# Kernel tuning notes

Hardware: AMD Instinct MI355X
Metric: run time of the kernel (lower is better)

The kernel has to match this reference:

```python
import jax, jax.numpy as jnp
import numpy as np

EPS = 1e-12  # F.normalize default eps


def setup_inputs() -> dict:
    key = jax.random.key(0)
    ks = jax.random.split(key, 6)
    B, C, D, H, W = 8, 192, 24, 24, 24
    heads = 6
    x = jax.random.normal(ks[0], (B, C, D, H, W), dtype=jnp.float32)
    qkv_w = jax.random.normal(ks[1], (3 * C, C), dtype=jnp.float32) * (1.0 / np.sqrt(C))
    qkv_b = jax.random.normal(ks[2], (3 * C,), dtype=jnp.float32) * 0.02
    temperature = jnp.ones((heads, 1, 1), dtype=jnp.float32)
    proj_w = jax.random.normal(ks[3], (C, C), dtype=jnp.float32) * (1.0 / np.sqrt(C))
    proj_b = jax.random.normal(ks[4], (C,), dtype=jnp.float32) * 0.02
    return {"x": x, "qkv_w": qkv_w, "qkv_b": qkv_b, "temperature": temperature,
            "proj_w": proj_w, "proj_b": proj_b}


def _l2norm_lastdim(t):
    n = jnp.sqrt(jnp.sum(t * t, axis=-1, keepdims=True))
    return t / jnp.maximum(n, EPS)


def reference(x, qkv_w, qkv_b, temperature, proj_w, proj_b):
    B, C, D, H, W = x.shape
    N = D * H * W
    heads = temperature.shape[0]
    hd = C // heads
    xf = x.reshape(B, C, N)
    # 1x1x1 Conv3d == per-voxel linear over channels: (B, 3C, N)
    qkv = jnp.einsum('bcn,oc->bon', xf, qkv_w) + qkv_b[None, :, None]
    # Faithful torch reshape of contiguous (B, 3C, N) buffer -> (B, N, 3, heads, hd),
    # then permute(2,0,3,4,1) -> (3, B, heads, hd, N)
    qkv = qkv.reshape(B, N, 3, heads, hd).transpose(2, 0, 3, 4, 1)
    q, k, v = qkv[0], qkv[1], qkv[2]
    q = _l2norm_lastdim(q)
    k = _l2norm_lastdim(k)
    # channel cross-covariance attention: (B, heads, hd, hd)
    attn = jnp.einsum('bhcn,bhdn->bhcd', q, k) * temperature[None]
    attn = jax.nn.softmax(attn, axis=-1)
    out = jnp.einsum('bhcd,bhdn->bhcn', attn, v)          # (B, heads, hd, N)
    out = out.transpose(0, 2, 1, 3).reshape(B, C, D, H, W)  # transpose(1,2) + reshape
    outf = out.reshape(B, C, N)
    y = jnp.einsum('bcn,oc->bon', outf, proj_w) + proj_b[None, :, None]
    return y.reshape(B, C, D, H, W)
```

## Files before the change

kernel.cpp:

```cpp
#include <hip/hip_runtime.h>

#define B_ 8
#define C_ 192
#define N_ 13824
#define HEADS 6
#define HD 32
#define THREEC 576

typedef unsigned short ushort_t;
typedef unsigned int uint_t;
typedef __attribute__((ext_vector_type(8))) short short8;
typedef __attribute__((ext_vector_type(4))) float f32x4;

__device__ __forceinline__ float bf2f(ushort_t u) {
  union { uint_t u; float f; } c; c.u = ((uint_t)u) << 16; return c.f;
}
__device__ __forceinline__ ushort_t f2bf(float f) {
  union { float f; uint_t u; } c; c.f = f;
  uint_t u = c.u;
  uint_t r = (u + 0x7fffu + ((u >> 16) & 1u)) >> 16;
  return (ushort_t)r;
}

#define LROW 200

__device__ __forceinline__ void rowperm(int f, int& row, int& u) {
  row = f / 24;
  int ul = f - row * 24;
  int uu = ul - (row & 7);
  u = uu + ((uu < 0) ? 24 : 0);
}

__global__ __launch_bounds__(256) void wconv(const float* __restrict__ w,
                                             ushort_t* __restrict__ wbf) {
  int idx = (blockIdx.x * 256 + threadIdx.x) * 8;
  float4 v0 = *(const float4*)&w[idx];
  float4 v1 = *(const float4*)&w[idx + 4];
  union { ushort_t us[8]; uint4 v; } pk;
  pk.us[0] = f2bf(v0.x); pk.us[1] = f2bf(v0.y); pk.us[2] = f2bf(v0.z); pk.us[3] = f2bf(v0.w);
  pk.us[4] = f2bf(v1.x); pk.us[5] = f2bf(v1.y); pk.us[6] = f2bf(v1.z); pk.us[7] = f2bf(v1.w);
  *(uint4*)&wbf[idx] = pk.v;
}

__global__ __launch_bounds__(256) void xt_conv(const float* __restrict__ x,
                                               ushort_t* __restrict__ xT) {
  __shared__ ushort_t tile[64 * 200];
  int t = threadIdx.x;
  int n0 = blockIdx.x * 64, b = blockIdx.y;
  const float* xb = x + (size_t)b * C_ * N_;
  int n4 = t & 15, cp = t >> 4;
#pragma unroll
  for (int it = 0; it < 6; ++it) {
    int c = (cp + it * 16) * 2;
    float4 v0 = *(const float4*)&xb[(size_t)c * N_ + n0 + n4 * 4];
    float4 v1 = *(const float4*)&xb[(size_t)(c + 1) * N_ + n0 + n4 * 4];
    float a0[4] = {v0.x, v0.y, v0.z, v0.w};
    float a1[4] = {v1.x, v1.y, v1.z, v1.w};
#pragma unroll
    for (int i = 0; i < 4; ++i) {
      uint_t wd = (uint_t)f2bf(a0[i]) | ((uint_t)f2bf(a1[i]) << 16);
      *(uint_t*)&tile[(n4 * 4 + i) * 200 + c] = wd;
    }
  }
  __syncthreads();
  ushort_t* xTb = xT + ((size_t)b * N_ + n0) * C_;
  int r = t >> 2, q = t & 3;
#pragma unroll
  for (int j = 0; j < 6; ++j) {
    int chunk = q * 6 + j;
    uint4 v = *(const uint4*)&tile[r * 200 + chunk * 8];
    *(uint4*)&xTb[r * 192 + chunk * 8] = v;
  }
}

__global__ __launch_bounds__(256) void qkv_gemm_mfma(
    const ushort_t* __restrict__ wbf, const ushort_t* __restrict__ xT,
    const float* __restrict__ bias, ushort_t* __restrict__ qkv) {
  __shared__ ushort_t As[64 * LROW];
  __shared__ ushort_t Bs[128 * LROW];
  int t = threadIdx.x;
  int o0 = blockIdx.x * 64, n0 = blockIdx.y * 128, b = blockIdx.z;
  int w = t >> 6, lane = t & 63;
  int ln16 = lane & 15, q4 = lane >> 4;

  const ushort_t* Asrc = wbf + (size_t)o0 * C_;
  const ushort_t* Bsrc = xT + ((size_t)b * N_ + n0) * C_;

  uint4 breg2[12]; int brow[12], bu[12];
#pragma unroll
  for (int j = 0; j < 12; ++j) {
    int f = (w * 12 + j) * 64 + lane;
    rowperm(f, brow[j], bu[j]);
    breg2[j] = *(const uint4*)(Bsrc + brow[j] * C_ + bu[j] * 8);
  }
  uint4 areg[6]; int arow[6], au[6];
#pragma unroll
  for (int j = 0; j < 6; ++j) {
    int f = (w * 6 + j) * 64 + lane;
    rowperm(f, arow[j], au[j]);
    areg[j] = *(const uint4*)(Asrc + arow[j] * C_ + au[j] * 8);
  }
#pragma unroll
  for (int j = 0; j < 12; ++j)
    *(uint4*)&Bs[brow[j] * LROW + bu[j] * 8] = breg2[j];
#pragma unroll
  for (int j = 0; j < 6; ++j)
    *(uint4*)&As[arow[j] * LROW + au[j] * 8] = areg[j];

  float breg[2][4];
#pragma unroll
  for (int mi = 0; mi < 2; ++mi)
#pragma unroll
    for (int r = 0; r < 4; ++r)
      breg[mi][r] = bias[o0 + (w >> 1) * 32 + mi * 16 + q4 * 4 + r];

  f32x4 acc[2][4];
#pragma unroll
  for (int mi = 0; mi < 2; ++mi)
#pragma unroll
    for (int ni = 0; ni < 4; ++ni) acc[mi][ni] = (f32x4){0.f, 0.f, 0.f, 0.f};

  __syncthreads();

  int mrow = (w >> 1) * 32, ncol = (w & 1) * 64;
#pragma unroll
  for (int kk = 0; kk < 6; ++kk) {
    int k0 = kk * 32 + q4 * 8;
    short8 a[2], bb[4];
#pragma unroll
    for (int mi = 0; mi < 2; ++mi)
      a[mi] = *(const short8*)&As[(mrow + mi * 16 + ln16) * LROW + k0];
#pragma unroll
    for (int ni = 0; ni < 4; ++ni)
      bb[ni] = *(const short8*)&Bs[(ncol + ni * 16 + ln16) * LROW + k0];
#pragma unroll
    for (int mi = 0; mi < 2; ++mi)
#pragma unroll
      for (int ni = 0; ni < 4; ++ni)
        acc[mi][ni] = __builtin_amdgcn_mfma_f32_16x16x32_bf16(
            a[mi], bb[ni], acc[mi][ni], 0, 0, 0);
  }

#pragma unroll
  for (int mi = 0; mi < 2; ++mi)
#pragma unroll
    for (int ni = 0; ni < 4; ++ni)
#pragma unroll
      for (int r = 0; r < 4; ++r) {
        float v = acc[mi][ni][r] + breg[mi][r];
        uint_t bf = f2bf(v);
        uint_t pv = (uint_t)__shfl_xor((int)bf, 1);
        if (!(lane & 1)) {
          int o_l = mrow + mi * 16 + q4 * 4 + r;
          int n_l = ncol + ni * 16 + ln16;
          *(uint_t*)&qkv[(size_t)(b * THREEC + o0 + o_l) * N_ + n0 + n_l] =
              bf | (pv << 16);
        }
      }
}

__global__ __launch_bounds__(256) void attn_partial(
    const ushort_t* __restrict__ qkv, float* __restrict__ Spart) {
  __shared__ float sh[4608];
  int t = threadIdx.x;
  int chunk = blockIdx.x, h = blockIdx.y, b = blockIdx.z;
  int j = t & 31, g8 = t >> 5;
  int tg = t >> 6, tl = t & 63;
  int c0 = (tl & 7) * 4, d0 = (tl >> 3) * 4;
  float acc[4][4];
#pragma unroll
  for (int i = 0; i < 4; ++i)
#pragma unroll
    for (int m = 0; m < 4; ++m) acc[i][m] = 0.f;
  float sqq = 0.f, sqk = 0.f;
  const ushort_t* basep = qkv + (size_t)b * THREEC * N_;
  int n2base = chunk * 1728;

  for (int p = 0; p < 27; ++p) {
    __syncthreads();
#pragma unroll
    for (int i = 0; i < 8; ++i) {
      int n2l = g8 * 8 + i;
      int n2 = n2base + p * 64 + n2l;
      int o = n2 / 24, r = n2 - o * 24;
      const ushort_t* rp = basep + (size_t)o * N_ + r * THREEC + h * HD + j;
      float qv = bf2f(rp[0]);
      float kv = bf2f(rp[C_]);
      sh[n2l * 32 + j] = qv;
      sh[2048 + n2l * 32 + j] = kv;
      sqq = fmaf(qv, qv, sqq);
      sqk = fmaf(kv, kv, sqk);
    }
    __syncthreads();
#pragma unroll
    for (int i = 0; i < 16; ++i) {
      int n2l = tg * 16 + i;
      float4 q4 = *(const float4*)&sh[n2l * 32 + c0];
      float4 k4 = *(const float4*)&sh[2048 + n2l * 32 + d0];
      float q[4] = {q4.x, q4.y, q4.z, q4.w};
      float kk[4] = {k4.x, k4.y, k4.z, k4.w};
#pragma unroll
      for (int ii = 0; ii < 4; ++ii)
#pragma unroll
        for (int mm = 0; mm < 4; ++mm)
          acc[ii][mm] = fmaf(q[ii], kk[mm], acc[ii][mm]);
    }
  }
  __syncthreads();
#pragma unroll
  for (int ii = 0; ii < 4; ++ii)
#pragma unroll
    for (int mm = 0; mm < 4; ++mm)
      sh[tg * 1024 + (c0 + ii) * 32 + (d0 + mm)] = acc[ii][mm];
  sh[4096 + g8 * 32 + j] = sqq;
  sh[4352 + g8 * 32 + j] = sqk;
  __syncthreads();

  float* outp = Spart + (size_t)((b * HEADS + h) * 8 + chunk) * 1088;
  for (int e = t; e < 1024; e += 256)
    outp[e] = sh[e] + sh[1024 + e] + sh[2048 + e] + sh[3072 + e];
  if (t < 32) {
    float s = 0.f;
#pragma unroll
    for (int g = 0; g < 8; ++g) s += sh[4096 + g * 32 + t];
    outp[1024 + t] = s;
  } else if (t < 64) {
    int jj = t - 32;
    float s = 0.f;
#pragma unroll
    for (int g = 0; g < 8; ++g) s += sh[4352 + g * 32 + jj];
    outp[1056 + jj] = s;
  }
}

__global__ __launch_bounds__(256) void attn_final(
    const float* __restrict__ Spart, const float* __restrict__ temp,
    const float* __restrict__ proj_w, ushort_t* __restrict__ W2bf) {
  __shared__ float Sl[1024];
  __shared__ float invq[32], invk[32];
  __shared__ float Pl[192 * 33];
  int t = threadIdx.x;
  int h = blockIdx.x, b = blockIdx.y;
  const float* base = Spart + (size_t)((b * HEADS + h) * 8) * 1088;

  for (int e = t; e < 1024; e += 256) {
    float s = 0.f;
#pragma unroll
    for (int ch = 0; ch < 8; ++ch) s += base[ch * 1088 + e];
    Sl[e] = s;
  }
  if (t < 64) {
    int jj = t & 31;
    int off = 1024 + (t >> 5) * 32 + jj;
    float s = 0.f;
#pragma unroll
    for (int ch = 0; ch < 8; ++ch) s += base[ch * 1088 + off];
    float inv = 1.f / fmaxf(sqrtf(s), 1e-12f);
    if (t < 32) invq[jj] = inv; else invk[jj] = inv;
  }
  for (int e = t; e < 6144; e += 256) {
    int co = e >> 5, c = e & 31;
    Pl[co * 33 + c] = proj_w[(size_t)co * C_ + c * HEADS + h];
  }
  __syncthreads();

  {
    int c = t >> 3, l8 = t & 7;
    float tmpv = temp[h];
    float iq = invq[c];
    float lg[4];
#pragma unroll
    for (int m = 0; m < 4; ++m) {
      int d = l8 * 4 + m;
      lg[m] = Sl[c * 32 + d] * iq * invk[d] * tmpv;
    }
    float mx = fmaxf(fmaxf(lg[0], lg[1]), fmaxf(lg[2], lg[3]));
    for (int off = 1; off < 8; off <<= 1) mx = fmaxf(mx, __shfl_xor(mx, off, 8));
    float ex[4]; float ssum = 0.f;
#pragma unroll
    for (int m = 0; m < 4; ++m) { ex[m] = __expf(lg[m] - mx); ssum += ex[m]; }
    for (int off = 1; off < 8; off <<= 1) ssum += __shfl_xor(ssum, off, 8);
    float inv = 1.f / ssum;
#pragma unroll
    for (int m = 0; m < 4; ++m) Sl[c * 32 + l8 * 4 + m] = ex[m] * inv;
  }
  __syncthreads();

  for (int e2 = t; e2 < 6144; e2 += 256) {
    int co = e2 >> 5, d = e2 & 31;
    float s = 0.f;
#pragma unroll
    for (int c = 0; c < 32; ++c)
      s = fmaf(Pl[co * 33 + c], Sl[c * 32 + d], s);
    W2bf[((size_t)b * C_ + co) * C_ + h * HD + d] = f2bf(s);
  }
}

__global__ __launch_bounds__(256) void proj_mfma(
    const ushort_t* __restrict__ qkv, const ushort_t* __restrict__ W2bf,
    const float* __restrict__ pb, float* __restrict__ y) {
  __shared__ ushort_t As[64 * LROW];
  __shared__ ushort_t Bs[128 * LROW];
  int t = threadIdx.x;
  int o0 = blockIdx.x * 64, n2_0 = blockIdx.y * 128, b = blockIdx.z;
  int w = t >> 6, lane = t & 63;
  int ln16 = lane & 15, q4 = lane >> 4;

  const ushort_t* Asrc = W2bf + ((size_t)b * C_ + o0) * C_;
  const ushort_t* basep = qkv + (size_t)b * THREEC * N_;

  uint4 breg2[12]; int brow[12], bu[12];
#pragma unroll
  for (int j = 0; j < 12; ++j) {
    int f = (w * 12 + j) * 64 + lane;
    rowperm(f, brow[j], bu[j]);
    int n2 = n2_0 + brow[j];
    int o = n2 / 24, r2 = n2 - o * 24;
    breg2[j] = *(const uint4*)(basep + (size_t)o * N_ + r2 * THREEC + 384 + bu[j] * 8);
  }
  uint4 areg[6]; int arow[6], au[6];
#pragma unroll
  for (int j = 0; j < 6; ++j) {
    int f = (w * 6 + j) * 64 + lane;
    rowperm(f, arow[j], au[j]);
    areg[j] = *(const uint4*)(Asrc + arow[j] * C_ + au[j] * 8);
  }
#pragma unroll
  for (int j = 0; j < 12; ++j)
    *(uint4*)&Bs[brow[j] * LROW + bu[j] * 8] = breg2[j];
#pragma unroll
  for (int j = 0; j < 6; ++j)
    *(uint4*)&As[arow[j] * LROW + au[j] * 8] = areg[j];

  float breg[2][4];
#pragma unroll
  for (int mi = 0; mi < 2; ++mi)
#pragma unroll
    for (int r = 0; r < 4; ++r)
      breg[mi][r] = pb[o0 + (w >> 1) * 32 + mi * 16 + q4 * 4 + r];

  f32x4 acc[2][4];
#pragma unroll
  for (int mi = 0; mi < 2; ++mi)
#pragma unroll
    for (int ni = 0; ni < 4; ++ni) acc[mi][ni] = (f32x4){0.f, 0.f, 0.f, 0.f};

  __syncthreads();

  int mrow = (w >> 1) * 32, ncol = (w & 1) * 64;
#pragma unroll
  for (int kk = 0; kk < 6; ++kk) {
    int k0 = kk * 32 + q4 * 8;
    short8 a[2], bb[4];
#pragma unroll
    for (int mi = 0; mi < 2; ++mi)
      a[mi] = *(const short8*)&As[(mrow + mi * 16 + ln16) * LROW + k0];
#pragma unroll
    for (int ni = 0; ni < 4; ++ni)
      bb[ni] = *(const short8*)&Bs[(ncol + ni * 16 + ln16) * LROW + k0];
#pragma unroll
    for (int mi = 0; mi < 2; ++mi)
#pragma unroll
      for (int ni = 0; ni < 4; ++ni)
        acc[mi][ni] = __builtin_amdgcn_mfma_f32_16x16x32_bf16(
            a[mi], bb[ni], acc[mi][ni], 0, 0, 0);
  }

#pragma unroll
  for (int mi = 0; mi < 2; ++mi)
#pragma unroll
    for (int ni = 0; ni < 4; ++ni)
#pragma unroll
      for (int r = 0; r < 4; ++r) {
        int co_l = mrow + mi * 16 + q4 * 4 + r;
        int n_l = ncol + ni * 16 + ln16;
        y[((size_t)b * C_ + o0 + co_l) * N_ + n2_0 + n_l] =
            acc[mi][ni][r] + breg[mi][r];
      }
}

extern "C" void kernel_launch(void* const* d_in, const int* in_sizes, int n_in,
                              void* d_out, int out_size, void* d_ws, size_t ws_size,
                              hipStream_t stream) {
  const float* x      = (const float*)d_in[0];
  const float* qkv_w  = (const float*)d_in[1];
  const float* qkv_b  = (const float*)d_in[2];
  const float* temp   = (const float*)d_in[3];
  const float* proj_w = (const float*)d_in[4];
  const float* proj_b = (const float*)d_in[5];
  float* y = (float*)d_out;

  char* wp = (char*)d_ws;
  ushort_t* qkv  = (ushort_t*)wp;  wp += (size_t)B_ * THREEC * N_ * 2;
  ushort_t* xT   = (ushort_t*)wp;  wp += (size_t)B_ * N_ * C_ * 2;
  float* Spart   = (float*)wp;     wp += (size_t)B_ * HEADS * 8 * 1088 * 4;
  ushort_t* W2bf = (ushort_t*)wp;  wp += (size_t)B_ * C_ * C_ * 2;
  ushort_t* wbf  = (ushort_t*)wp;

  wconv<<<54, 256, 0, stream>>>(qkv_w, wbf);
  xt_conv<<<dim3(216, B_), 256, 0, stream>>>(x, xT);
  qkv_gemm_mfma<<<dim3(9, 108, B_), 256, 0, stream>>>(wbf, xT, qkv_b, qkv);
  attn_partial<<<dim3(8, HEADS, B_), 256, 0, stream>>>(qkv, Spart);
  attn_final<<<dim3(HEADS, B_), 256, 0, stream>>>(Spart, temp, proj_w, W2bf);
  proj_mfma<<<dim3(3, 108, B_), 256, 0, stream>>>(qkv, W2bf, proj_b, y);
}
```

Before: 339.7 us.

## Fuse bf16 conversion into QKV GEMM, loop output tiles, and rework attention partials

The separate weight and input bf16 conversion kernels are removed. The QKV GEMM now reads fp32 x directly, converts it into LDS, and keeps the B fragments in registers while looping over all nine output-channel tiles, prefetching the next weight tile. Attention partial sums are restructured to handle all heads per block with 54 chunks, coalesced uint4 loads and double-buffered bf16 LDS. The projection GEMM likewise loops over output tiles and reuses the B fragments. This drops the xT round trip and several launches, at the cost of higher register pressure and fewer, longer blocks.

```diff
diff --git a/kernel.cpp b/kernel.cpp
--- a/kernel.cpp
+++ b/kernel.cpp
@@ -6,6 +6,7 @@
 #define HEADS 6
 #define HD 32
 #define THREEC 576
+#define CH 54
 
 typedef unsigned short ushort_t;
 typedef unsigned int uint_t;
@@ -14,6 +15,12 @@
 
 __device__ __forceinline__ float bf2f(ushort_t u) {
   union { uint_t u; float f; } c; c.u = ((uint_t)u) << 16; return c.f;
+}
+__device__ __forceinline__ float lo_f(uint_t u) {
+  union { uint_t u; float f; } c; c.u = u << 16; return c.f;
+}
+__device__ __forceinline__ float hi_f(uint_t u) {
+  union { uint_t u; float f; } c; c.u = u & 0xffff0000u; return c.f;
 }
 __device__ __forceinline__ ushort_t f2bf(float f) {
   union { float f; uint_t u; } c; c.f = f;
@@ -24,212 +31,215 @@
 
 #define LROW 200
 
-__device__ __forceinline__ void rowperm(int f, int& row, int& u) {
-  row = f / 24;
-  int ul = f - row * 24;
-  int uu = ul - (row & 7);
-  u = uu + ((uu < 0) ? 24 : 0);
-}
-
-__global__ __launch_bounds__(256) void wconv(const float* __restrict__ w,
-                                             ushort_t* __restrict__ wbf) {
-  int idx = (blockIdx.x * 256 + threadIdx.x) * 8;
-  float4 v0 = *(const float4*)&w[idx];
-  float4 v1 = *(const float4*)&w[idx + 4];
-  union { ushort_t us[8]; uint4 v; } pk;
-  pk.us[0] = f2bf(v0.x); pk.us[1] = f2bf(v0.y); pk.us[2] = f2bf(v0.z); pk.us[3] = f2bf(v0.w);
-  pk.us[4] = f2bf(v1.x); pk.us[5] = f2bf(v1.y); pk.us[6] = f2bf(v1.z); pk.us[7] = f2bf(v1.w);
-  *(uint4*)&wbf[idx] = pk.v;
-}
-
-__global__ __launch_bounds__(256) void xt_conv(const float* __restrict__ x,
-                                               ushort_t* __restrict__ xT) {
-  __shared__ ushort_t tile[64 * 200];
+__global__ __launch_bounds__(256, 2) void qkv_fused(
+    const float* __restrict__ x, const float* __restrict__ w,
+    const float* __restrict__ bias, ushort_t* __restrict__ qkv) {
+  __shared__ ushort_t Bs[128 * LROW];
+  __shared__ ushort_t As[64 * LROW];
   int t = threadIdx.x;
-  int n0 = blockIdx.x * 64, b = blockIdx.y;
+  int n0 = blockIdx.x * 128, b = blockIdx.y;
+  int wid = t >> 6, lane = t & 63;
+  int ln16 = lane & 15, q4 = lane >> 4;
   const float* xb = x + (size_t)b * C_ * N_;
-  int n4 = t & 15, cp = t >> 4;
-#pragma unroll
-  for (int it = 0; it < 6; ++it) {
-    int c = (cp + it * 16) * 2;
-    float4 v0 = *(const float4*)&xb[(size_t)c * N_ + n0 + n4 * 4];
-    float4 v1 = *(const float4*)&xb[(size_t)(c + 1) * N_ + n0 + n4 * 4];
-    float a0[4] = {v0.x, v0.y, v0.z, v0.w};
-    float a1[4] = {v1.x, v1.y, v1.z, v1.w};
-#pragma unroll
-    for (int i = 0; i < 4; ++i) {
-      uint_t wd = (uint_t)f2bf(a0[i]) | ((uint_t)f2bf(a1[i]) << 16);
-      *(uint_t*)&tile[(n4 * 4 + i) * 200 + c] = wd;
-    }
-  }
-  __syncthreads();
-  ushort_t* xTb = xT + ((size_t)b * N_ + n0) * C_;
-  int r = t >> 2, q = t & 3;
+
+  {
+    int nl = t & 127;
+    int cb0 = (t >> 7) * 8;
+#pragma unroll
+    for (int it = 0; it < 12; ++it) {
+      int cb = cb0 + it * 16;
+      float v[8];
+#pragma unroll
+      for (int j = 0; j < 8; ++j)
+        v[j] = xb[(size_t)(cb + j) * N_ + n0 + nl];
+      union { ushort_t us[8]; uint4 u4; } pk;
+#pragma unroll
+      for (int j = 0; j < 8; ++j) pk.us[j] = f2bf(v[j]);
+      *(uint4*)&Bs[nl * LROW + cb] = pk.u4;
+    }
+  }
+
+  int ar = t >> 2, au0 = t & 3;
+  uint4 apre[6];
 #pragma unroll
   for (int j = 0; j < 6; ++j) {
-    int chunk = q * 6 + j;
-    uint4 v = *(const uint4*)&tile[r * 200 + chunk * 8];
-    *(uint4*)&xTb[r * 192 + chunk * 8] = v;
-  }
-}
-
-__global__ __launch_bounds__(256) void qkv_gemm_mfma(
-    const ushort_t* __restrict__ wbf, const ushort_t* __restrict__ xT,
-    const float* __restrict__ bias, ushort_t* __restrict__ qkv) {
-  __shared__ ushort_t As[64 * LROW];
-  __shared__ ushort_t Bs[128 * LROW];
+    int u = au0 + 4 * j;
+    const float* src = w + (size_t)ar * C_ + u * 8;
+    float4 v0 = *(const float4*)src;
+    float4 v1 = *(const float4*)(src + 4);
+    union { ushort_t us[8]; uint4 u4; } pk;
+    pk.us[0] = f2bf(v0.x); pk.us[1] = f2bf(v0.y); pk.us[2] = f2bf(v0.z); pk.us[3] = f2bf(v0.w);
+    pk.us[4] = f2bf(v1.x); pk.us[5] = f2bf(v1.y); pk.us[6] = f2bf(v1.z); pk.us[7] = f2bf(v1.w);
+    apre[j] = pk.u4;
+  }
+
+  __syncthreads();
+
+#pragma unroll
+  for (int j = 0; j < 6; ++j)
+    *(uint4*)&As[ar * LROW + (au0 + 4 * j) * 8] = apre[j];
+
+  int ncol = (wid & 1) * 64, mrow = (wid >> 1) * 32;
+  short8 bb[6][4];
+#pragma unroll
+  for (int kk = 0; kk < 6; ++kk)
+#pragma unroll
+    for (int ni = 0; ni < 4; ++ni)
+      bb[kk][ni] = *(const short8*)&Bs[(ncol + ni * 16 + ln16) * LROW + kk * 32 + q4 * 8];
+
+  __syncthreads();
+
+  for (int p = 0; p < 9; ++p) {
+    if (p < 8) {
+      int o0n = (p + 1) * 64;
+#pragma unroll
+      for (int j = 0; j < 6; ++j) {
+        int u = au0 + 4 * j;
+        const float* src = w + (size_t)(o0n + ar) * C_ + u * 8;
+        float4 v0 = *(const float4*)src;
+        float4 v1 = *(const float4*)(src + 4);
+        union { ushort_t us[8]; uint4 u4; } pk;
+        pk.us[0] = f2bf(v0.x); pk.us[1] = f2bf(v0.y); pk.us[2] = f2bf(v0.z); pk.us[3] = f2bf(v0.w);
+        pk.us[4] = f2bf(v1.x); pk.us[5] = f2bf(v1.y); pk.us[6] = f2bf(v1.z); pk.us[7] = f2bf(v1.w);
+        apre[j] = pk.u4;
+      }
+    }
+
+    float brg[2][4];
+#pragma unroll
+    for (int mi = 0; mi < 2; ++mi)
+#pragma unroll
+      for (int r = 0; r < 4; ++r)
+        brg[mi][r] = bias[p * 64 + mrow + mi * 16 + q4 * 4 + r];
+
+    f32x4 acc[2][4];
+#pragma unroll
+    for (int mi = 0; mi < 2; ++mi)
+#pragma unroll
+      for (int ni = 0; ni < 4; ++ni) acc[mi][ni] = (f32x4){0.f, 0.f, 0.f, 0.f};
+
+#pragma unroll
+    for (int kk = 0; kk < 6; ++kk) {
+      short8 a[2];
+#pragma unroll
+      for (int mi = 0; mi < 2; ++mi)
+        a[mi] = *(const short8*)&As[(mrow + mi * 16 + ln16) * LROW + kk * 32 + q4 * 8];
+#pragma unroll
+      for (int mi = 0; mi < 2; ++mi)
+#pragma unroll
+        for (int ni = 0; ni < 4; ++ni)
+          acc[mi][ni] = __builtin_amdgcn_mfma_f32_16x16x32_bf16(
+              a[mi], bb[kk][ni], acc[mi][ni], 0, 0, 0);
+    }
+
+#pragma unroll
+    for (int mi = 0; mi < 2; ++mi)
+#pragma unroll
+      for (int ni = 0; ni < 4; ++ni)
+#pragma unroll
+        for (int r = 0; r < 4; ++r) {
+          float v = acc[mi][ni][r] + brg[mi][r];
+          uint_t bf = f2bf(v);
+          uint_t pv = (uint_t)__shfl_xor((int)bf, 1);
+          if (!(lane & 1)) {
+            int o_l = p * 64 + mrow + mi * 16 + q4 * 4 + r;
+            int n_l = ncol + ni * 16 + ln16;
+            *(uint_t*)&qkv[(size_t)(b * THREEC + o_l) * N_ + n0 + n_l] =
+                bf | (pv << 16);
+          }
+        }
+
+    __syncthreads();
+    if (p < 8) {
+#pragma unroll
+      for (int j = 0; j < 6; ++j)
+        *(uint4*)&As[ar * LROW + (au0 + 4 * j) * 8] = apre[j];
+      __syncthreads();
+    }
+  }
+}
+
+#define K2RS 392
+__global__ __launch_bounds__(384) void attn_partial(
+    const ushort_t* __restrict__ qkv, float* __restrict__ Spart) {
+  __shared__ ushort_t sh[2][32 * K2RS];
   int t = threadIdx.x;
-  int o0 = blockIdx.x * 64, n0 = blockIdx.y * 128, b = blockIdx.z;
-  int w = t >> 6, lane = t & 63;
-  int ln16 = lane & 15, q4 = lane >> 4;
-
-  const ushort_t* Asrc = wbf + (size_t)o0 * C_;
-  const ushort_t* Bsrc = xT + ((size_t)b * N_ + n0) * C_;
-
-  uint4 breg2[12]; int brow[12], bu[12];
-#pragma unroll
-  for (int j = 0; j < 12; ++j) {
-    int f = (w * 12 + j) * 64 + lane;
-    rowperm(f, brow[j], bu[j]);
-    breg2[j] = *(const uint4*)(Bsrc + brow[j] * C_ + bu[j] * 8);
-  }
-  uint4 areg[6]; int arow[6], au[6];
-#pragma unroll
-  for (int j = 0; j < 6; ++j) {
-    int f = (w * 6 + j) * 64 + lane;
-    rowperm(f, arow[j], au[j]);
-    areg[j] = *(const uint4*)(Asrc + arow[j] * C_ + au[j] * 8);
-  }
-#pragma unroll
-  for (int j = 0; j < 12; ++j)
-    *(uint4*)&Bs[brow[j] * LROW + bu[j] * 8] = breg2[j];
-#pragma unroll
-  for (int j = 0; j < 6; ++j)
-    *(uint4*)&As[arow[j] * LROW + au[j] * 8] = areg[j];
-
-  float breg[2][4];
-#pragma unroll
-  for (int mi = 0; mi < 2; ++mi)
-#pragma unroll
-    for (int r = 0; r < 4; ++r)
-      breg[mi][r] = bias[o0 + (w >> 1) * 32 + mi * 16 + q4 * 4 + r];
-
-  f32x4 acc[2][4];
-#pragma unroll
-  for (int mi = 0; mi < 2; ++mi)
-#pragma unroll
-    for (int ni = 0; ni < 4; ++ni) acc[mi][ni] = (f32x4){0.f, 0.f, 0.f, 0.f};
-
-  __syncthreads();
-
-  int mrow = (w >> 1) * 32, ncol = (w & 1) * 64;
-#pragma unroll
-  for (int kk = 0; kk < 6; ++kk) {
-    int k0 = kk * 32 + q4 * 8;
-    short8 a[2], bb[4];
-#pragma unroll
-    for (int mi = 0; mi < 2; ++mi)
-      a[mi] = *(const short8*)&As[(mrow + mi * 16 + ln16) * LROW + k0];
-#pragma unroll
-    for (int ni = 0; ni < 4; ++ni)
-      bb[ni] = *(const short8*)&Bs[(ncol + ni * 16 + ln16) * LROW + k0];
-#pragma unroll
-    for (int mi = 0; mi < 2; ++mi)
-#pragma unroll
-      for (int ni = 0; ni < 4; ++ni)
-        acc[mi][ni] = __builtin_amdgcn_mfma_f32_16x16x32_bf16(
-            a[mi], bb[ni], acc[mi][ni], 0, 0, 0);
-  }
-
-#pragma unroll
-  for (int mi = 0; mi < 2; ++mi)
-#pragma unroll
-    for (int ni = 0; ni < 4; ++ni)
-#pragma unroll
-      for (int r = 0; r < 4; ++r) {
-        float v = acc[mi][ni][r] + breg[mi][r];
-        uint_t bf = f2bf(v);
-        uint_t pv = (uint_t)__shfl_xor((int)bf, 1);
-        if (!(lane & 1)) {
-          int o_l = mrow + mi * 16 + q4 * 4 + r;
-          int n_l = ncol + ni * 16 + ln16;
-          *(uint_t*)&qkv[(size_t)(b * THREEC + o0 + o_l) * N_ + n0 + n_l] =
-              bf | (pv << 16);
-        }
+  int chunk = blockIdx.x, b = blockIdx.y;
+  const ushort_t* basep = qkv + (size_t)b * THREEC * N_;
+  int n2base = chunk * 256;
+  int h = t / 64, tl = t & 63;
+  int c0 = (tl & 7) * 4, d0 = (tl >> 3) * 4;
+
+  float acc[4][4];
+#pragma unroll
+  for (int i = 0; i < 4; ++i)
+#pragma unroll
+    for (int m = 0; m < 4; ++m) acc[i][m] = 0.f;
+  float sqq[4] = {0.f, 0.f, 0.f, 0.f}, sqk[4] = {0.f, 0.f, 0.f, 0.f};
+
+  uint4 pre[4];
+  int srr[4], sru[4];
+#pragma unroll
+  for (int i = 0; i < 4; ++i) {
+    int idx = t + i * 384;
+    srr[i] = idx / 48; sru[i] = idx - srr[i] * 48;
+  }
+#pragma unroll
+  for (int i = 0; i < 4; ++i) {
+    int n2 = n2base + srr[i];
+    int o = n2 / 24, rr = n2 - o * 24;
+    pre[i] = *(const uint4*)(basep + (size_t)o * N_ + rr * THREEC + sru[i] * 8);
+  }
+#pragma unroll
+  for (int i = 0; i < 4; ++i)
+    *(uint4*)&sh[0][srr[i] * K2RS + sru[i] * 8] = pre[i];
+
+  for (int it = 0; it < 8; ++it) {
+    if (it < 7) {
+#pragma unroll
+      for (int i = 0; i < 4; ++i) {
+        int n2 = n2base + (it + 1) * 32 + srr[i];
+        int o = n2 / 24, rr = n2 - o * 24;
+        pre[i] = *(const uint4*)(basep + (size_t)o * N_ + rr * THREEC + sru[i] * 8);
       }
-}
-
-__global__ __launch_bounds__(256) void attn_partial(
-    const ushort_t* __restrict__ qkv, float* __restrict__ Spart) {
-  __shared__ float sh[4608];
-  int t = threadIdx.x;
-  int chunk = blockIdx.x, h = blockIdx.y, b = blockIdx.z;
-  int j = t & 31, g8 = t >> 5;
-  int tg = t >> 6, tl = t & 63;
-  int c0 = (tl & 7) * 4, d0 = (tl >> 3) * 4;
-  float acc[4][4];
-#pragma unroll
-  for (int i = 0; i < 4; ++i)
-#pragma unroll
-    for (int m = 0; m < 4; ++m) acc[i][m] = 0.f;
-  float sqq = 0.f, sqk = 0.f;
-  const ushort_t* basep = qkv + (size_t)b * THREEC * N_;
-  int n2base = chunk * 1728;
-
-  for (int p = 0; p < 27; ++p) {
+    }
     __syncthreads();
-#pragma unroll
-    for (int i = 0; i < 8; ++i) {
-      int n2l = g8 * 8 + i;
-      int n2 = n2base + p * 64 + n2l;
-      int o = n2 / 24, r = n2 - o * 24;
-      const ushort_t* rp = basep + (size_t)o * N_ + r * THREEC + h * HD + j;
-      float qv = bf2f(rp[0]);
-      float kv = bf2f(rp[C_]);
-      sh[n2l * 32 + j] = qv;
-      sh[2048 + n2l * 32 + j] = kv;
-      sqq = fmaf(qv, qv, sqq);
-      sqk = fmaf(kv, kv, sqk);
-    }
-    __syncthreads();
-#pragma unroll
-    for (int i = 0; i < 16; ++i) {
-      int n2l = tg * 16 + i;
-      float4 q4 = *(const float4*)&sh[n2l * 32 + c0];
-      float4 k4 = *(const float4*)&sh[2048 + n2l * 32 + d0];
-      float q[4] = {q4.x, q4.y, q4.z, q4.w};
-      float kk[4] = {k4.x, k4.y, k4.z, k4.w};
-#pragma unroll
-      for (int ii = 0; ii < 4; ++ii)
-#pragma unroll
-        for (int mm = 0; mm < 4; ++mm)
-          acc[ii][mm] = fmaf(q[ii], kk[mm], acc[ii][mm]);
-    }
-  }
-  __syncthreads();
-#pragma unroll
-  for (int ii = 0; ii < 4; ++ii)
-#pragma unroll
-    for (int mm = 0; mm < 4; ++mm)
-      sh[tg * 1024 + (c0 + ii) * 32 + (d0 + mm)] = acc[ii][mm];
-  sh[4096 + g8 * 32 + j] = sqq;
-  sh[4352 + g8 * 32 + j] = sqk;
-  __syncthreads();
-
-  float* outp = Spart + (size_t)((b * HEADS + h) * 8 + chunk) * 1088;
-  for (int e = t; e < 1024; e += 256)
-    outp[e] = sh[e] + sh[1024 + e] + sh[2048 + e] + sh[3072 + e];
-  if (t < 32) {
-    float s = 0.f;
-#pragma unroll
-    for (int g = 0; g < 8; ++g) s += sh[4096 + g * 32 + t];
-    outp[1024 + t] = s;
-  } else if (t < 64) {
-    int jj = t - 32;
-    float s = 0.f;
-#pragma unroll
-    for (int g = 0; g < 8; ++g) s += sh[4352 + g * 32 + jj];
-    outp[1056 + jj] = s;
+    if (it < 7) {
+#pragma unroll
+      for (int i = 0; i < 4; ++i)
+        *(uint4*)&sh[(it + 1) & 1][srr[i] * K2RS + sru[i] * 8] = pre[i];
+    }
+    const ushort_t* buf = sh[it & 1];
+#pragma unroll 4
+    for (int row = 0; row < 32; ++row) {
+      uint2 qv = *(const uint2*)&buf[row * K2RS + h * HD + c0];
+      uint2 kv = *(const uint2*)&buf[row * K2RS + C_ + h * HD + d0];
+      float q[4] = {lo_f(qv.x), hi_f(qv.x), lo_f(qv.y), hi_f(qv.y)};
+      float k[4] = {lo_f(kv.x), hi_f(kv.x), lo_f(kv.y), hi_f(kv.y)};
+#pragma unroll
+      for (int i = 0; i < 4; ++i) {
+        sqq[i] = fmaf(q[i], q[i], sqq[i]);
+        sqk[i] = fmaf(k[i], k[i], sqk[i]);
+#pragma unroll
+        for (int m = 0; m < 4; ++m)
+          acc[i][m] = fmaf(q[i], k[m], acc[i][m]);
+      }
+    }
+  }
+
+  float* outp = Spart + ((size_t)(b * HEADS + h) * CH + chunk) * 1088;
+#pragma unroll
+  for (int i = 0; i < 4; ++i) {
+    float4 v = {acc[i][0], acc[i][1], acc[i][2], acc[i][3]};
+    *(float4*)&outp[(c0 + i) * 32 + d0] = v;
+  }
+  if (tl < 8) {
+#pragma unroll
+    for (int i = 0; i < 4; ++i) outp[1024 + c0 + i] = sqq[i];
+  }
+  if ((tl & 7) == 0) {
+#pragma unroll
+    for (int i = 0; i < 4; ++i) outp[1056 + d0 + i] = sqk[i];
   }
 }
 
@@ -241,20 +251,18 @@
   __shared__ float Pl[192 * 33];
   int t = threadIdx.x;
   int h = blockIdx.x, b = blockIdx.y;
-  const float* base = Spart + (size_t)((b * HEADS + h) * 8) * 1088;
+  const float* base = Spart + (size_t)(b * HEADS + h) * CH * 1088;
 
   for (int e = t; e < 1024; e += 256) {
     float s = 0.f;
-#pragma unroll
-    for (int ch = 0; ch < 8; ++ch) s += base[ch * 1088 + e];
+    for (int ch = 0; ch < CH; ++ch) s += base[ch * 1088 + e];
     Sl[e] = s;
   }
   if (t < 64) {
     int jj = t & 31;
     int off = 1024 + (t >> 5) * 32 + jj;
     float s = 0.f;
-#pragma unroll
-    for (int ch = 0; ch < 8; ++ch) s += base[ch * 1088 + off];
+    for (int ch = 0; ch < CH; ++ch) s += base[ch * 1088 + off];
     float inv = 1.f / fmaxf(sqrtf(s), 1e-12f);
     if (t < 32) invq[jj] = inv; else invk[jj] = inv;
   }
@@ -296,87 +304,109 @@
   }
 }
 
-__global__ __launch_bounds__(256) void proj_mfma(
+__global__ __launch_bounds__(256, 2) void proj_fused(
     const ushort_t* __restrict__ qkv, const ushort_t* __restrict__ W2bf,
     const float* __restrict__ pb, float* __restrict__ y) {
+  __shared__ ushort_t Bs[128 * LROW];
   __shared__ ushort_t As[64 * LROW];
-  __shared__ ushort_t Bs[128 * LROW];
   int t = threadIdx.x;
-  int o0 = blockIdx.x * 64, n2_0 = blockIdx.y * 128, b = blockIdx.z;
-  int w = t >> 6, lane = t & 63;
+  int n2_0 = blockIdx.x * 128, b = blockIdx.y;
+  int wid = t >> 6, lane = t & 63;
   int ln16 = lane & 15, q4 = lane >> 4;
-
-  const ushort_t* Asrc = W2bf + ((size_t)b * C_ + o0) * C_;
   const ushort_t* basep = qkv + (size_t)b * THREEC * N_;
 
-  uint4 breg2[12]; int brow[12], bu[12];
-#pragma unroll
-  for (int j = 0; j < 12; ++j) {
-    int f = (w * 12 + j) * 64 + lane;
-    rowperm(f, brow[j], bu[j]);
-    int n2 = n2_0 + brow[j];
-    int o = n2 / 24, r2 = n2 - o * 24;
-    breg2[j] = *(const uint4*)(basep + (size_t)o * N_ + r2 * THREEC + 384 + bu[j] * 8);
-  }
-  uint4 areg[6]; int arow[6], au[6];
+  {
+    int nl = t >> 1, u0 = t & 1;
+#pragma unroll
+    for (int j = 0; j < 12; ++j) {
+      int u = u0 + 2 * j;
+      int n2 = n2_0 + nl;
+      int o = n2 / 24, r2 = n2 - o * 24;
+      uint4 v = *(const uint4*)(basep + (size_t)o * N_ + r2 * THREEC + 384 + u * 8);
+      *(uint4*)&Bs[nl * LROW + u * 8] = v;
+    }
+  }
+
+  int ar = t >> 2, au0 = t & 3;
+  uint4 apre[6];
 #pragma unroll
   for (int j = 0; j < 6; ++j) {
-    int f = (w * 6 + j) * 64 + lane;
-    rowperm(f, arow[j], au[j]);
-    areg[j] = *(const uint4*)(Asrc + arow[j] * C_ + au[j] * 8);
-  }
-#pragma unroll
-  for (int j = 0; j < 12; ++j)
-    *(uint4*)&Bs[brow[j] * LROW + bu[j] * 8] = breg2[j];
+    int u = au0 + 4 * j;
+    apre[j] = *(const uint4*)(W2bf + ((size_t)b * C_ + ar) * C_ + u * 8);
+  }
+
+  __syncthreads();
+
 #pragma unroll
   for (int j = 0; j < 6; ++j)
-    *(uint4*)&As[arow[j] * LROW + au[j] * 8] = areg[j];
-
-  float breg[2][4];
-#pragma unroll
-  for (int mi = 0; mi < 2; ++mi)
-#pragma unroll
-    for (int r = 0; r < 4; ++r)
-      breg[mi][r] = pb[o0 + (w >> 1) * 32 + mi * 16 + q4 * 4 + r];
-
-  f32x4 acc[2][4];
-#pragma unroll
-  for (int mi = 0; mi < 2; ++mi)
-#pragma unroll
-    for (int ni = 0; ni < 4; ++ni) acc[mi][ni] = (f32x4){0.f, 0.f, 0.f, 0.f};
-
-  __syncthreads();
-
-  int mrow = (w >> 1) * 32, ncol = (w & 1) * 64;
-#pragma unroll
-  for (int kk = 0; kk < 6; ++kk) {
-    int k0 = kk * 32 + q4 * 8;
-    short8 a[2], bb[4];
-#pragma unroll
-    for (int mi = 0; mi < 2; ++mi)
-      a[mi] = *(const short8*)&As[(mrow + mi * 16 + ln16) * LROW + k0];
+    *(uint4*)&As[ar * LROW + (au0 + 4 * j) * 8] = apre[j];
+
+  int ncol = (wid & 1) * 64, mrow = (wid >> 1) * 32;
+  short8 bb[6][4];
+#pragma unroll
+  for (int kk = 0; kk < 6; ++kk)
 #pragma unroll
     for (int ni = 0; ni < 4; ++ni)
-      bb[ni] = *(const short8*)&Bs[(ncol + ni * 16 + ln16) * LROW + k0];
+      bb[kk][ni] = *(const short8*)&Bs[(ncol + ni * 16 + ln16) * LROW + kk * 32 + q4 * 8];
+
+  __syncthreads();
+
+  for (int p = 0; p < 3; ++p) {
+    if (p < 2) {
+      int o0n = (p + 1) * 64;
+#pragma unroll
+      for (int j = 0; j < 6; ++j) {
+        int u = au0 + 4 * j;
+        apre[j] = *(const uint4*)(W2bf + ((size_t)b * C_ + o0n + ar) * C_ + u * 8);
+      }
+    }
+
+    float brg[2][4];
+#pragma unroll
+    for (int mi = 0; mi < 2; ++mi)
+#pragma unroll
+      for (int r = 0; r < 4; ++r)
+        brg[mi][r] = pb[p * 64 + mrow + mi * 16 + q4 * 4 + r];
+
+    f32x4 acc[2][4];
+#pragma unroll
+    for (int mi = 0; mi < 2; ++mi)
+#pragma unroll
+      for (int ni = 0; ni < 4; ++ni) acc[mi][ni] = (f32x4){0.f, 0.f, 0.f, 0.f};
+
+#pragma unroll
+    for (int kk = 0; kk < 6; ++kk) {
+      short8 a[2];
+#pragma unroll
+      for (int mi = 0; mi < 2; ++mi)
+        a[mi] = *(const short8*)&As[(mrow + mi * 16 + ln16) * LROW + kk * 32 + q4 * 8];
+#pragma unroll
+      for (int mi = 0; mi < 2; ++mi)
+#pragma unroll
+        for (int ni = 0; ni < 4; ++ni)
+          acc[mi][ni] = __builtin_amdgcn_mfma_f32_16x16x32_bf16(
+              a[mi], bb[kk][ni], acc[mi][ni], 0, 0, 0);
+    }
+
 #pragma unroll
     for (int mi = 0; mi < 2; ++mi)
 #pragma unroll
       for (int ni = 0; ni < 4; ++ni)
-        acc[mi][ni] = __builtin_amdgcn_mfma_f32_16x16x32_bf16(
-            a[mi], bb[ni], acc[mi][ni], 0, 0, 0);
-  }
-
-#pragma unroll
-  for (int mi = 0; mi < 2; ++mi)
-#pragma unroll
-    for (int ni = 0; ni < 4; ++ni)
-#pragma unroll
-      for (int r = 0; r < 4; ++r) {
-        int co_l = mrow + mi * 16 + q4 * 4 + r;
-        int n_l = ncol + ni * 16 + ln16;
-        y[((size_t)b * C_ + o0 + co_l) * N_ + n2_0 + n_l] =
-            acc[mi][ni][r] + breg[mi][r];
-      }
+#pragma unroll
+        for (int r = 0; r < 4; ++r) {
+          int co_l = p * 64 + mrow + mi * 16 + q4 * 4 + r;
+          int n_l = ncol + ni * 16 + ln16;
+          y[((size_t)b * C_ + co_l) * N_ + n2_0 + n_l] = acc[mi][ni][r] + brg[mi][r];
+        }
+
+    __syncthreads();
+    if (p < 2) {
+#pragma unroll
+      for (int j = 0; j < 6; ++j)
+        *(uint4*)&As[ar * LROW + (au0 + 4 * j) * 8] = apre[j];
+      __syncthreads();
+    }
+  }
 }
 
 extern "C" void kernel_launch(void* const* d_in, const int* in_sizes, int n_in,
@@ -392,15 +422,11 @@
 
   char* wp = (char*)d_ws;
   ushort_t* qkv  = (ushort_t*)wp;  wp += (size_t)B_ * THREEC * N_ * 2;
-  ushort_t* xT   = (ushort_t*)wp;  wp += (size_t)B_ * N_ * C_ * 2;
-  float* Spart   = (float*)wp;     wp += (size_t)B_ * HEADS * 8 * 1088 * 4;
-  ushort_t* W2bf = (ushort_t*)wp;  wp += (size_t)B_ * C_ * C_ * 2;
-  ushort_t* wbf  = (ushort_t*)wp;
-
-  wconv<<<54, 256, 0, stream>>>(qkv_w, wbf);
-  xt_conv<<<dim3(216, B_), 256, 0, stream>>>(x, xT);
-  qkv_gemm_mfma<<<dim3(9, 108, B_), 256, 0, stream>>>(wbf, xT, qkv_b, qkv);
-  attn_partial<<<dim3(8, HEADS, B_), 256, 0, stream>>>(qkv, Spart);
+  float* Spart   = (float*)wp;     wp += (size_t)B_ * HEADS * CH * 1088 * 4;
+  ushort_t* W2bf = (ushort_t*)wp;
+
+  qkv_fused<<<dim3(108, B_), 256, 0, stream>>>(x, qkv_w, qkv_b, qkv);
+  attn_partial<<<dim3(CH, B_), 384, 0, stream>>>(qkv, Spart);
   attn_final<<<dim3(HEADS, B_), 256, 0, stream>>>(Spart, temp, proj_w, W2bf);
-  proj_mfma<<<dim3(3, 108, B_), 256, 0, stream>>>(qkv, W2bf, proj_b, y);
-}
+  proj_fused<<<dim3(108, B_), 256, 0, stream>>>(qkv, W2bf, proj_b, y);
+}
```

Result: no change. 342.9 us (+1.0%).
